# Performance work log

Measured on AMD Instinct MI355X. Metric: run time of the kernel, lower is better.

The kernel has to match this reference:

```python
import jax, jax.numpy as jnp
import numpy as np

V = 30000
Y = 30000
D = 768
B = 8
N = 512
PAD_ID = 0
POS_EXPONENT = 1
NEG_INF = 1e12
LN_EPS = 1e-5


def setup_inputs() -> dict:
    key = jax.random.key(0)
    k1, k2, k3, k4, k5 = jax.random.split(key, 5)
    M_s = jax.random.randint(k1, (B, N), 0, V, dtype=jnp.int64)
    E_v = jax.random.normal(k2, (V, D), dtype=jnp.float32) * 0.02
    E_y = jax.random.normal(k3, (Y, D), dtype=jnp.float32) * 0.02
    # padding_idx=0 -> zero rows
    E_v = E_v.at[PAD_ID].set(0.0)
    E_y = E_y.at[PAD_ID].set(0.0)
    W_A = jax.random.normal(k4, (D, D), dtype=jnp.float32) * (1.0 / np.sqrt(D))
    W_O = jax.random.normal(k5, (D, D), dtype=jnp.float32) * (1.0 / np.sqrt(D))
    gamma = jnp.ones((D,), dtype=jnp.float32)
    beta = jnp.zeros((D,), dtype=jnp.float32)
    return {"M_s": M_s, "E_v": E_v, "E_y": E_y, "W_A": W_A, "W_O": W_O,
            "gamma": gamma, "beta": beta}


def positional_rep(seq_len: int, exponent: int) -> jnp.ndarray:
    idx = jnp.arange(seq_len)
    rel = (idx[None, :] - idx[:, None]).astype(jnp.float32)  # [N, N], j - i
    sign = jnp.where(rel >= 0, 1.0, -1.0)
    return sign * jnp.abs(rel) ** exponent


def layer_norm(x, gamma, beta):
    mu = jnp.mean(x, axis=-1, keepdims=True)
    var = jnp.mean((x - mu) ** 2, axis=-1, keepdims=True)
    return (x - mu) * jax.lax.rsqrt(var + LN_EPS) * gamma + beta


def reference(M_s, E_v, E_y, W_A, W_O, gamma, beta):
    # Embedding lookup (dropout is identity at eval / p=0)
    X = E_v[M_s]                                   # [B, N, D]
    Q = X                                          # self-attention mode (v_q=None)
    mask = (M_s != PAD_ID)                         # [B, N]

    # attention: logits = (Q @ W_A) @ X^T + pos_bias, mask, softmax
    logits = jnp.einsum('bnd,bmd->bnm', Q @ W_A, X)  # [B, N, N]
    logits = logits + positional_rep(X.shape[1], POS_EXPONENT)[None]
    logits = jnp.where(mask[:, None, :], logits, -NEG_INF)
    A = jax.nn.softmax(logits, axis=-1)            # [B, N, N]
    Q_c = jnp.einsum('bnm,bmd->bnd', A, X @ W_O)   # [B, N, D]

    H = layer_norm(Q_c + Q, gamma, beta)           # [B, N, D]
    y_logits = jnp.einsum('bnd,yd->bny', H, E_y)   # [B, N, Y]
    return y_logits, A
```

## Files before the change

### kernel.cpp

```cpp
#include <hip/hip_runtime.h>
#include <hip/hip_bf16.h>

using bf16 = __hip_bfloat16;
typedef __attribute__((ext_vector_type(8))) short bf16x8;
typedef __attribute__((ext_vector_type(4))) float f32x4;

#define DEV __device__ __forceinline__

#define AS1 __attribute__((address_space(1)))
#define AS3 __attribute__((address_space(3)))
#define SB  __builtin_amdgcn_sched_barrier(0)
#define BARR __builtin_amdgcn_s_barrier()
#define LG0 asm volatile("s_waitcnt lgkmcnt(0)" ::: "memory")
#define VM3 asm volatile("s_waitcnt vmcnt(3)" ::: "memory")
#define VM1 asm volatile("s_waitcnt vmcnt(1)" ::: "memory")
#define VM0 asm volatile("s_waitcnt vmcnt(0)" ::: "memory")

static constexpr int Bsz = 8, Nseq = 512, Dm = 768, Vv = 30000, Yv = 30000;
static constexpr int Ypad = 30208;
static constexpr int Tok = Bsz * Nseq;
static constexpr int NT = Dm / 32;

__global__ __launch_bounds__(512, 4)
void gemm_big(const bf16* __restrict__ Ag, const bf16* __restrict__ Bg,
              float* __restrict__ Cg)
{
    __shared__ bf16 sm[6][4096];

    int bid = blockIdx.x;
    { int cpx = gridDim.x >> 3; bid = (bid & 7) * cpx + (bid >> 3); }
    const int mT = bid & 31;
    const int nT = bid >> 5;

    const int tid  = threadIdx.x;
    const int lane = tid & 63;
    const int wid  = tid >> 6;
    const int wm   = wid >> 2;
    const int wn   = wid & 3;

    const int lr = tid >> 2;
    const int sc = ((tid & 3) ^ (lr & 3)) << 3;
    const bf16* aS  = Ag + (long)(mT * 128 + lr) * Dm + sc;
    const bf16* bS0 = Bg + (long)(nT * 256 + lr) * Dm + sc;
    const bf16* bS1 = bS0 + (long)128 * Dm;
    const int ldsW = wid << 9;

    const int fl = lane & 15;
    const int fh = lane >> 4;
    const int e0 = (fh ^ (fl & 3)) << 3;
    const int aro = (wm * 64 + fl) * 32;
    const int bro = (wn * 32 + fl) * 32;

    bf16x8 afr[4], bfr[2];
    f32x4 acc[4][2][2] = {};

#define STG(CI, PTR, T)                                                        \
    __builtin_amdgcn_global_load_lds((const AS1 void*)((PTR) + (T) * 32),      \
        (AS3 void*)&sm[CI][ldsW], 16, 0, 0);
#define RA(CI)                                                                 \
    _Pragma("unroll") for (int mm = 0; mm < 4; ++mm)                           \
        afr[mm] = *(const bf16x8*)&sm[CI][aro + mm * 512 + e0];
#define RB(CI)                                                                 \
    _Pragma("unroll") for (int nn = 0; nn < 2; ++nn)                           \
        bfr[nn] = *(const bf16x8*)&sm[CI][bro + nn * 512 + e0];
#define MF8(NQ)                                                                \
    __builtin_amdgcn_s_setprio(1);                                             \
    _Pragma("unroll") for (int mm = 0; mm < 4; ++mm)                           \
    _Pragma("unroll") for (int nn = 0; nn < 2; ++nn)                           \
        acc[mm][NQ][nn] = __builtin_amdgcn_mfma_f32_16x16x32_bf16(             \
            afr[mm], bfr[nn], acc[mm][NQ][nn], 0, 0, 0);                       \
    __builtin_amdgcn_s_setprio(0);

    STG(0, aS, 0) STG(1, bS0, 0) STG(2, bS1, 0) STG(3, aS, 1) STG(4, bS0, 1)
    VM3; SB; BARR; SB;

#pragma unroll 1
    for (int t = 0; t < NT - 2; t += 2) {
        RA(0) RB(1)
        STG(5, bS1, t + 1)
        VM3; SB; BARR; LG0; SB;
        MF8(0)
        SB; BARR; SB;
        RB(2)
        STG(0, aS, t + 2) STG(1, bS0, t + 2)
        VM3; SB; BARR; LG0; SB;
        MF8(1)
        SB; BARR; SB;
        RA(3) RB(4)
        STG(2, bS1, t + 2)
        VM3; SB; BARR; LG0; SB;
        MF8(0)
        SB; BARR; SB;
        RB(5)
        STG(3, aS, t + 3) STG(4, bS0, t + 3)
        VM3; SB; BARR; LG0; SB;
        MF8(1)
        SB; BARR; SB;
    }

    {
        RA(0) RB(1)
        STG(5, bS1, NT - 1)
        VM3; SB; BARR; LG0; SB;
        MF8(0)
        SB; BARR; SB;
        RB(2)
        VM1; SB; BARR; LG0; SB;
        MF8(1)
        SB; BARR; SB;
        RA(3) RB(4)
        VM0; SB; BARR; LG0; SB;
        MF8(0)
        SB; BARR; SB;
        RB(5)
        SB; BARR; LG0; SB;
        MF8(1)
    }

    const int rB = mT * 128 + wm * 64 + fh * 4;
    const int cB = nT * 256 + wn * 32 + fl;
#pragma unroll
    for (int mm = 0; mm < 4; ++mm)
#pragma unroll
    for (int nq = 0; nq < 2; ++nq)
#pragma unroll
    for (int nn = 0; nn < 2; ++nn) {
        const int c = cB + nq * 128 + nn * 16;
        if (c >= Yv) continue;
        const int r = rB + mm * 16;
#pragma unroll
        for (int j = 0; j < 4; ++j)
            __builtin_nontemporal_store(acc[mm][nq][nn][j],
                                        Cg + (long)(r + j) * Yv + c);
    }
#undef STG
#undef RA
#undef RB
#undef MF8
}

template<bool STORE_BF16>
__global__ __launch_bounds__(256)
void gemm_bt(const bf16* __restrict__ Ag, const bf16* __restrict__ Bg,
             void* __restrict__ Cg, int M, int Nc, int K, int lda, int ldc,
             long sA, long sB, long sC)
{
    __shared__ bf16 As[128 * 32];
    __shared__ bf16 Bs[128 * 32];

    const int bz = blockIdx.z;
    const bf16* A  = Ag + (long)bz * sA;
    const bf16* Bm = Bg + (long)bz * sB;

    const int bid = blockIdx.x;
    const int nTilesM = M >> 7;
    const int mTile = bid % nTilesM;
    const int nTile = bid / nTilesM;

    const int tid  = threadIdx.x;
    const int wave = tid >> 6;
    const int lane = tid & 63;

    const int sRow = (wave << 4) + (lane >> 2);
    const int sCol = (lane & 3) << 3;

    const long aBase = (long)(mTile * 128) * lda;
    const long bBase = (long)(nTile * 128) * K;

    const int fl = lane & 15;
    const int fh = lane >> 4;
    const int wRow = (wave >> 1) << 6;
    const int wCol = (wave & 1) << 6;

    f32x4 acc[4][4] = {};

    for (int k0 = 0; k0 < K; k0 += 32) {
#pragma unroll
        for (int t = 0; t < 2; ++t) {
            const bf16* gA = A  + aBase + (long)(t * 64 + sRow) * lda + (k0 + sCol);
            const bf16* gB = Bm + bBase + (long)(t * 64 + sRow) * K + (k0 + sCol);
            bf16* lA = &As[(t * 64 + (wave << 4)) * 32];
            bf16* lB = &Bs[(t * 64 + (wave << 4)) * 32];
            __builtin_amdgcn_global_load_lds(
                (const AS1 void*)gA, (AS3 void*)lA, 16, 0, 0);
            __builtin_amdgcn_global_load_lds(
                (const AS1 void*)gB, (AS3 void*)lB, 16, 0, 0);
        }
        __syncthreads();

        bf16x8 af[4], bfg[4];
#pragma unroll
        for (int m = 0; m < 4; ++m)
            af[m] = *(const bf16x8*)&As[(wRow + m * 16 + fl) * 32 + fh * 8];
#pragma unroll
        for (int n = 0; n < 4; ++n)
            bfg[n] = *(const bf16x8*)&Bs[(wCol + n * 16 + fl) * 32 + fh * 8];
#pragma unroll
        for (int m = 0; m < 4; ++m)
#pragma unroll
            for (int n = 0; n < 4; ++n)
                acc[m][n] = __builtin_amdgcn_mfma_f32_16x16x32_bf16(
                    af[m], bfg[n], acc[m][n], 0, 0, 0);
        __syncthreads();
    }

    const int rBase = mTile * 128 + wRow + fh * 4;
    const int cBase = nTile * 128 + wCol + fl;
#pragma unroll
    for (int m = 0; m < 4; ++m) {
#pragma unroll
        for (int n = 0; n < 4; ++n) {
            int gc = cBase + n * 16;
            int gr = rBase + m * 16;
            if (STORE_BF16) {
                bf16* C = (bf16*)Cg + (long)bz * sC;
#pragma unroll
                for (int j = 0; j < 4; ++j)
                    C[(long)(gr + j) * ldc + gc] = __float2bfloat16(acc[m][n][j]);
            } else {
                float* C = (float*)Cg + (long)bz * sC;
#pragma unroll
                for (int j = 0; j < 4; ++j)
                    C[(long)(gr + j) * ldc + gc] = acc[m][n][j];
            }
        }
    }
}

__global__ __launch_bounds__(256)
void gemm_bt64(const bf16* __restrict__ Ag, const bf16* __restrict__ Bg,
               bf16* __restrict__ Cg, int M, int K, int lda, int ldc,
               long sA, long sB, long sC)
{
    __shared__ bf16 As[64 * 32];
    __shared__ bf16 Bs[128 * 32];

    const int bz = blockIdx.z;
    const bf16* A  = Ag + (long)bz * sA;
    const bf16* Bm = Bg + (long)bz * sB;
    bf16* C = Cg + (long)bz * sC;

    const int bid = blockIdx.x;
    const int nTilesM = M >> 6;
    const int mTile = bid % nTilesM;
    const int nTile = bid / nTilesM;

    const int tid  = threadIdx.x;
    const int wave = tid >> 6;
    const int lane = tid & 63;

    const int sRow = tid >> 2;
    const int sCol = (tid & 3) << 3;

    const long aBase = (long)(mTile * 64) * lda;
    const long bBase = (long)(nTile * 128) * K;

    const int fl = lane & 15;
    const int fh = lane >> 4;

    f32x4 acc[4][2] = {};

    for (int k0 = 0; k0 < K; k0 += 32) {
        __builtin_amdgcn_global_load_lds(
            (const AS1 void*)(A + aBase + (long)sRow * lda + (k0 + sCol)),
            (AS3 void*)&As[wave * 512], 16, 0, 0);
#pragma unroll
        for (int t = 0; t < 2; ++t)
            __builtin_amdgcn_global_load_lds(
                (const AS1 void*)(Bm + bBase + (long)(t * 64 + sRow) * K + (k0 + sCol)),
                (AS3 void*)&Bs[t * 2048 + wave * 512], 16, 0, 0);
        __syncthreads();

        bf16x8 af[4], bfg[2];
#pragma unroll
        for (int m = 0; m < 4; ++m)
            af[m] = *(const bf16x8*)&As[(m * 16 + fl) * 32 + fh * 8];
#pragma unroll
        for (int n = 0; n < 2; ++n)
            bfg[n] = *(const bf16x8*)&Bs[(wave * 32 + n * 16 + fl) * 32 + fh * 8];
#pragma unroll
        for (int m = 0; m < 4; ++m)
#pragma unroll
            for (int n = 0; n < 2; ++n)
                acc[m][n] = __builtin_amdgcn_mfma_f32_16x16x32_bf16(
                    af[m], bfg[n], acc[m][n], 0, 0, 0);
        __syncthreads();
    }

    const int rBase = mTile * 64 + fh * 4;
    const int cBase = nTile * 128 + wave * 32 + fl;
#pragma unroll
    for (int m = 0; m < 4; ++m)
#pragma unroll
    for (int n = 0; n < 2; ++n) {
        const int gc = cBase + n * 16;
        const int gr = rBase + m * 16;
#pragma unroll
        for (int j = 0; j < 4; ++j)
            C[(long)(gr + j) * ldc + gc] = __float2bfloat16(acc[m][n][j]);
    }
}

static constexpr int PREP_CVT = 11328, PREP_WT = 1152, PREP_GATHER = 4096;

__global__ __launch_bounds__(256)
void k_prep(const float* __restrict__ Ey, bf16* __restrict__ Eyb,
            const float* __restrict__ WA, const float* __restrict__ WO,
            bf16* __restrict__ Wcat,
            const int* __restrict__ Ms, const float* __restrict__ Ev,
            bf16* __restrict__ Xb)
{
    __shared__ float t[32][33];
    const int b = blockIdx.x;
    const int tid = threadIdx.x;

    if (b < PREP_CVT) {
        const long idx = ((long)b * 256 + tid) * 8;
        const int row = (int)(idx / Dm);
        union { bf16 h[8]; uint4 u; } pk;
        if (row < Yv) {
            const f32x4* s = (const f32x4*)(Ey + idx);
            f32x4 a = __builtin_nontemporal_load(s);
            f32x4 c = __builtin_nontemporal_load(s + 1);
#pragma unroll
            for (int i = 0; i < 4; ++i) {
                pk.h[i]     = __float2bfloat16(a[i]);
                pk.h[4 + i] = __float2bfloat16(c[i]);
            }
        } else {
#pragma unroll
            for (int i = 0; i < 8; ++i) pk.h[i] = __float2bfloat16(0.f);
        }
        *(uint4*)(Eyb + idx) = pk.u;
    } else if (b < PREP_CVT + PREP_WT) {
        const int rem = b - PREP_CVT;
        const int z = rem / 576, r2 = rem % 576;
        const int bx = (r2 % 24) * 32, by = (r2 / 24) * 32;
        const float* W = z ? WO : WA;
        bf16* WT = Wcat + (size_t)z * Dm * Dm;
        const int tx = tid & 31, ty = tid >> 5;
#pragma unroll
        for (int i = 0; i < 32; i += 8)
            t[ty + i][tx] = W[(long)(bx + ty + i) * Dm + (by + tx)];
        __syncthreads();
#pragma unroll
        for (int i = 0; i < 32; i += 8)
            WT[(long)(by + ty + i) * Dm + (bx + tx)] = __float2bfloat16(t[tx][ty + i]);
    } else {
        const int token = b - (PREP_CVT + PREP_WT);
        if (tid < 192) {
            const int id = Ms[token];
            const int d = tid * 4;
            float4 v = *(const float4*)(Ev + (long)id * Dm + d);
            union { bf16 h[4]; uint2 u; } pk;
            pk.h[0] = __float2bfloat16(v.x); pk.h[1] = __float2bfloat16(v.y);
            pk.h[2] = __float2bfloat16(v.z); pk.h[3] = __float2bfloat16(v.w);
            *(uint2*)(Xb + (long)token * Dm + d) = pk.u;
        }
    }
}

__global__ void k_xwoT(const bf16* __restrict__ Xo, bf16* __restrict__ XoT)
{
    __shared__ bf16 t[32][33];
    int b = blockIdx.z;
    const bf16* src = Xo + (long)b * Nseq * 1536 + 768;
    bf16* dst = XoT + (long)b * Dm * Nseq;
    int bx = blockIdx.x * 32;
    int by = blockIdx.y * 32;
    int tx = threadIdx.x, ty = threadIdx.y;
#pragma unroll
    for (int i = 0; i < 32; i += 8)
        t[ty + i][tx] = src[(long)(bx + ty + i) * 1536 + (by + tx)];
    __syncthreads();
#pragma unroll
    for (int i = 0; i < 32; i += 8)
        dst[(long)(by + ty + i) * Nseq + (bx + tx)] = t[tx][ty + i];
}

DEV float waveMax(float v) {
#pragma unroll
    for (int o = 32; o > 0; o >>= 1) v = fmaxf(v, __shfl_xor(v, o, 64));
    return v;
}
DEV float waveSum(float v) {
#pragma unroll
    for (int o = 32; o > 0; o >>= 1) v += __shfl_xor(v, o, 64);
    return v;
}

__global__ __launch_bounds__(256) void k_softmax(const bf16* __restrict__ L,
                                                 const int* __restrict__ Ms,
                                                 float* __restrict__ Aout,
                                                 bf16* __restrict__ Ab)
{
    __shared__ float red[8];
    int row = blockIdx.x;
    int b = row >> 9, i = row & 511;
    const bf16* l = L + (long)row * Nseq;
    const int* ms = Ms + (b << 9);
    int t = threadIdx.x;
    int wid = t >> 6, lane = t & 63;
    int j0 = t, j1 = t + 256;

    float a0 = __bfloat162float(l[j0]) + (float)(j0 - i);
    float a1 = __bfloat162float(l[j1]) + (float)(j1 - i);
    if (ms[j0] == 0) a0 = -1e12f;
    if (ms[j1] == 0) a1 = -1e12f;

    float m = waveMax(fmaxf(a0, a1));
    if (lane == 0) red[wid] = m;
    __syncthreads();
    m = fmaxf(fmaxf(red[0], red[1]), fmaxf(red[2], red[3]));

    float e0 = expf(a0 - m), e1 = expf(a1 - m);
    float s = waveSum(e0 + e1);
    if (lane == 0) red[4 + wid] = s;
    __syncthreads();
    s = red[4] + red[5] + red[6] + red[7];
    float inv = 1.0f / s;

    float r0 = e0 * inv, r1 = e1 * inv;
    __builtin_nontemporal_store(r0, &Aout[(long)row * Nseq + j0]);
    __builtin_nontemporal_store(r1, &Aout[(long)row * Nseq + j1]);
    Ab[(long)row * Nseq + j0] = __float2bfloat16(r0);
    Ab[(long)row * Nseq + j1] = __float2bfloat16(r1);
}

__global__ __launch_bounds__(256) void k_ln(const float* __restrict__ Qc,
                                            const bf16* __restrict__ Xb,
                                            const float* __restrict__ gamma,
                                            const float* __restrict__ beta,
                                            bf16* __restrict__ Hb)
{
    __shared__ float red[8];
    int row = blockIdx.x;
    const float* q = Qc + (long)row * Dm;
    const bf16* e = Xb + (long)row * Dm;
    int t = threadIdx.x;
    int wid = t >> 6, lane = t & 63;

    float x[3];
#pragma unroll
    for (int c = 0; c < 3; ++c)
        x[c] = q[t + c * 256] + __bfloat162float(e[t + c * 256]);

    float s = waveSum(x[0] + x[1] + x[2]);
    if (lane == 0) red[wid] = s;
    __syncthreads();
    float mu = (red[0] + red[1] + red[2] + red[3]) * (1.0f / 768.0f);

    float vs = 0.f;
#pragma unroll
    for (int c = 0; c < 3; ++c) { float d = x[c] - mu; vs += d * d; }
    vs = waveSum(vs);
    if (lane == 0) red[4 + wid] = vs;
    __syncthreads();
    float var = (red[4] + red[5] + red[6] + red[7]) * (1.0f / 768.0f);
    float rstd = rsqrtf(var + 1e-5f);

#pragma unroll
    for (int c = 0; c < 3; ++c) {
        int d = t + c * 256;
        Hb[(long)row * Dm + d] =
            __float2bfloat16((x[c] - mu) * rstd * gamma[d] + beta[d]);
    }
}

extern "C" void kernel_launch(void* const* d_in, const int* in_sizes, int n_in,
                              void* d_out, int out_size, void* d_ws, size_t ws_size,
                              hipStream_t stream)
{
    const int*   Ms    = (const int*)d_in[0];
    const float* Ev    = (const float*)d_in[1];
    const float* Ey    = (const float*)d_in[2];
    const float* WA    = (const float*)d_in[3];
    const float* WO    = (const float*)d_in[4];
    const float* gamma = (const float*)d_in[5];
    const float* beta  = (const float*)d_in[6];

    float* y_out = (float*)d_out;
    float* A_out = y_out + (size_t)Tok * Yv;

    char* ws = (char*)d_ws;
    size_t off = 0;
    auto alloc = [&](size_t n) { char* p = ws + off; off += (n + 255) & ~(size_t)255; return p; };
    bf16*  Xb    = (bf16*) alloc((size_t)Tok * Dm * 2);
    bf16*  WcatT = (bf16*) alloc((size_t)2 * Dm * Dm * 2);
    bf16*  QXWb  = (bf16*) alloc((size_t)Tok * 1536 * 2);
    bf16*  XWobT = (bf16*) alloc((size_t)Tok * Dm * 2);
    bf16*  Lb    = (bf16*) alloc((size_t)Tok * Nseq * 2);
    bf16*  Ab    = (bf16*) alloc((size_t)Tok * Nseq * 2);
    float* Qc    = (float*)alloc((size_t)Tok * Dm * 4);
    bf16*  Hb    = (bf16*) alloc((size_t)Tok * Dm * 2);
    bf16*  Eyb   = (bf16*) alloc((size_t)Ypad * Dm * 2);

    k_prep<<<dim3(PREP_CVT + PREP_WT + PREP_GATHER), dim3(256), 0, stream>>>(
        Ey, Eyb, WA, WO, WcatT, Ms, Ev, Xb);
    gemm_bt<true><<<dim3(384), dim3(256), 0, stream>>>(
        Xb, WcatT, (void*)QXWb, Tok, 1536, Dm, Dm, 1536, 0L, 0L, 0L);
    gemm_bt64<<<dim3(32, 1, 8), dim3(256), 0, stream>>>(
        QXWb, Xb, Lb, Nseq, Dm, 1536, Nseq,
        (long)Nseq * 1536, (long)Nseq * Dm, (long)Nseq * Nseq);
    k_softmax<<<dim3(Tok), dim3(256), 0, stream>>>(Lb, Ms, A_out, Ab);
    k_xwoT<<<dim3(16, 24, 8), dim3(32, 8), 0, stream>>>(QXWb, XWobT);
    gemm_bt<false><<<dim3(24, 1, 8), dim3(256), 0, stream>>>(
        Ab, XWobT, (void*)Qc, Nseq, Dm, Nseq, Nseq, Dm,
        (long)Nseq * Nseq, (long)Dm * Nseq, (long)Nseq * Dm);
    k_ln<<<dim3(Tok), dim3(256), 0, stream>>>(Qc, Xb, gamma, beta, Hb);
    gemm_big<<<dim3(32 * (Ypad / 256)), dim3(512), 0, stream>>>(Hb, Eyb, y_out);
}
```

Before: 350.1 us.

## Produce X·W_O transposed directly via swapped GEMM and store Q_c in bf16

The fused QW/XWo projection GEMM is split into two GEMMs. The second computes Wo^T·X^T so its output is already laid out transposed, which removes the separate k_xwoT transpose kernel and its extra read and write pass. gemm_bt gains an explicit ldb so it can read B strided per batch. The attention-output GEMM now stores Q_c in bf16 instead of fp32, halving that intermediate's traffic into layer norm at some cost in precision.

```diff
diff --git a/kernel.cpp b/kernel.cpp
--- a/kernel.cpp
+++ b/kernel.cpp
@@ -142,8 +142,8 @@
 template<bool STORE_BF16>
 __global__ __launch_bounds__(256)
 void gemm_bt(const bf16* __restrict__ Ag, const bf16* __restrict__ Bg,
-             void* __restrict__ Cg, int M, int Nc, int K, int lda, int ldc,
-             long sA, long sB, long sC)
+             void* __restrict__ Cg, int M, int Nc, int K,
+             int lda, int ldb, int ldc, long sA, long sB, long sC)
 {
     __shared__ bf16 As[128 * 32];
     __shared__ bf16 Bs[128 * 32];
@@ -165,7 +165,7 @@
     const int sCol = (lane & 3) << 3;
 
     const long aBase = (long)(mTile * 128) * lda;
-    const long bBase = (long)(nTile * 128) * K;
+    const long bBase = (long)(nTile * 128) * ldb;
 
     const int fl = lane & 15;
     const int fh = lane >> 4;
@@ -178,7 +178,7 @@
 #pragma unroll
         for (int t = 0; t < 2; ++t) {
             const bf16* gA = A  + aBase + (long)(t * 64 + sRow) * lda + (k0 + sCol);
-            const bf16* gB = Bm + bBase + (long)(t * 64 + sRow) * K + (k0 + sCol);
+            const bf16* gB = Bm + bBase + (long)(t * 64 + sRow) * ldb + (k0 + sCol);
             bf16* lA = &As[(t * 64 + (wave << 4)) * 32];
             bf16* lB = &Bs[(t * 64 + (wave << 4)) * 32];
             __builtin_amdgcn_global_load_lds(
@@ -360,24 +360,6 @@
     }
 }
 
-__global__ void k_xwoT(const bf16* __restrict__ Xo, bf16* __restrict__ XoT)
-{
-    __shared__ bf16 t[32][33];
-    int b = blockIdx.z;
-    const bf16* src = Xo + (long)b * Nseq * 1536 + 768;
-    bf16* dst = XoT + (long)b * Dm * Nseq;
-    int bx = blockIdx.x * 32;
-    int by = blockIdx.y * 32;
-    int tx = threadIdx.x, ty = threadIdx.y;
-#pragma unroll
-    for (int i = 0; i < 32; i += 8)
-        t[ty + i][tx] = src[(long)(bx + ty + i) * 1536 + (by + tx)];
-    __syncthreads();
-#pragma unroll
-    for (int i = 0; i < 32; i += 8)
-        dst[(long)(by + ty + i) * Nseq + (bx + tx)] = t[tx][ty + i];
-}
-
 DEV float waveMax(float v) {
 #pragma unroll
     for (int o = 32; o > 0; o >>= 1) v = fmaxf(v, __shfl_xor(v, o, 64));
@@ -427,7 +409,7 @@
     Ab[(long)row * Nseq + j1] = __float2bfloat16(r1);
 }
 
-__global__ __launch_bounds__(256) void k_ln(const float* __restrict__ Qc,
+__global__ __launch_bounds__(256) void k_ln(const bf16* __restrict__ Qc,
                                             const bf16* __restrict__ Xb,
                                             const float* __restrict__ gamma,
                                             const float* __restrict__ beta,
@@ -435,7 +417,7 @@
 {
     __shared__ float red[8];
     int row = blockIdx.x;
-    const float* q = Qc + (long)row * Dm;
+    const bf16* q = Qc + (long)row * Dm;
     const bf16* e = Xb + (long)row * Dm;
     int t = threadIdx.x;
     int wid = t >> 6, lane = t & 63;
@@ -443,7 +425,7 @@
     float x[3];
 #pragma unroll
     for (int c = 0; c < 3; ++c)
-        x[c] = q[t + c * 256] + __bfloat162float(e[t + c * 256]);
+        x[c] = __bfloat162float(q[t + c * 256]) + __bfloat162float(e[t + c * 256]);
 
     float s = waveSum(x[0] + x[1] + x[2]);
     if (lane == 0) red[wid] = s;
@@ -487,26 +469,28 @@
     auto alloc = [&](size_t n) { char* p = ws + off; off += (n + 255) & ~(size_t)255; return p; };
     bf16*  Xb    = (bf16*) alloc((size_t)Tok * Dm * 2);
     bf16*  WcatT = (bf16*) alloc((size_t)2 * Dm * Dm * 2);
-    bf16*  QXWb  = (bf16*) alloc((size_t)Tok * 1536 * 2);
-    bf16*  XWobT = (bf16*) alloc((size_t)Tok * Dm * 2);
+    bf16*  QWb   = (bf16*) alloc((size_t)Tok * Dm * 2);
+    bf16*  XWoT  = (bf16*) alloc((size_t)Dm * Tok * 2);
     bf16*  Lb    = (bf16*) alloc((size_t)Tok * Nseq * 2);
     bf16*  Ab    = (bf16*) alloc((size_t)Tok * Nseq * 2);
-    float* Qc    = (float*)alloc((size_t)Tok * Dm * 4);
+    bf16*  Qcb   = (bf16*) alloc((size_t)Tok * Dm * 2);
     bf16*  Hb    = (bf16*) alloc((size_t)Tok * Dm * 2);
     bf16*  Eyb   = (bf16*) alloc((size_t)Ypad * Dm * 2);
 
     k_prep<<<dim3(PREP_CVT + PREP_WT + PREP_GATHER), dim3(256), 0, stream>>>(
         Ey, Eyb, WA, WO, WcatT, Ms, Ev, Xb);
-    gemm_bt<true><<<dim3(384), dim3(256), 0, stream>>>(
-        Xb, WcatT, (void*)QXWb, Tok, 1536, Dm, Dm, 1536, 0L, 0L, 0L);
+    gemm_bt<true><<<dim3(192), dim3(256), 0, stream>>>(
+        Xb, WcatT, (void*)QWb, Tok, Dm, Dm, Dm, Dm, Dm, 0L, 0L, 0L);
+    gemm_bt<true><<<dim3(192), dim3(256), 0, stream>>>(
+        WcatT + (size_t)Dm * Dm, Xb, (void*)XWoT, Dm, Tok, Dm, Dm, Dm, Tok,
+        0L, 0L, 0L);
     gemm_bt64<<<dim3(32, 1, 8), dim3(256), 0, stream>>>(
-        QXWb, Xb, Lb, Nseq, Dm, 1536, Nseq,
-        (long)Nseq * 1536, (long)Nseq * Dm, (long)Nseq * Nseq);
+        QWb, Xb, Lb, Nseq, Dm, Dm, Nseq,
+        (long)Nseq * Dm, (long)Nseq * Dm, (long)Nseq * Nseq);
     k_softmax<<<dim3(Tok), dim3(256), 0, stream>>>(Lb, Ms, A_out, Ab);
-    k_xwoT<<<dim3(16, 24, 8), dim3(32, 8), 0, stream>>>(QXWb, XWobT);
-    gemm_bt<false><<<dim3(24, 1, 8), dim3(256), 0, stream>>>(
-        Ab, XWobT, (void*)Qc, Nseq, Dm, Nseq, Nseq, Dm,
-        (long)Nseq * Nseq, (long)Dm * Nseq, (long)Nseq * Dm);
-    k_ln<<<dim3(Tok), dim3(256), 0, stream>>>(Qc, Xb, gamma, beta, Hb);
+    gemm_bt<true><<<dim3(24, 1, 8), dim3(256), 0, stream>>>(
+        Ab, XWoT, (void*)Qcb, Nseq, Dm, Nseq, Nseq, Tok, Dm,
+        (long)Nseq * Nseq, (long)Nseq, (long)Nseq * Dm);
+    k_ln<<<dim3(Tok), dim3(256), 0, stream>>>(Qcb, Xb, gamma, beta, Hb);
     gemm_big<<<dim3(32 * (Ypad / 256)), dim3(512), 0, stream>>>(Hb, Eyb, y_out);
 }
```

Measured after the change: 364.7 us. 4.2% more time.
